# Kernel optimization log

Hardware: AMD Instinct MI355X
Metric: run time of the kernel (lower is better)

Reference implementation:

```python
import jax, jax.numpy as jnp
import numpy as np

NUM_HEADS = 16
WINDOW = 128  # local-attention half-width used by the mask generator
NEG_INF = -1e9


def setup_inputs() -> dict:
    key = jax.random.key(0)
    ks = jax.random.split(key, 12)
    T, N, C = 2048, 2, 1024
    s = 1.0 / np.sqrt(C)
    inp = {
        "q": jax.random.normal(ks[0], (T, N, C), jnp.float32),
        "k": jax.random.normal(ks[1], (T, N, C), jnp.float32),
        "v": jax.random.normal(ks[2], (T, N, C), jnp.float32),
        # MultiHeadDispatch: separate q/k/v input projections + output projection (with bias)
        "Wq": jax.random.normal(ks[3], (C, C), jnp.float32) * s,
        "bq": jnp.zeros((C,), jnp.float32),
        "Wk": jax.random.normal(ks[4], (C, C), jnp.float32) * s,
        "bk": jnp.zeros((C,), jnp.float32),
        "Wv": jax.random.normal(ks[5], (C, C), jnp.float32) * s,
        "bv": jnp.zeros((C,), jnp.float32),
        "Wo": jax.random.normal(ks[6], (C, C), jnp.float32) * s,
        "bo": jnp.zeros((C,), jnp.float32),
        "key_length": jax.random.randint(ks[7], (N,), 1, T, dtype=jnp.int32),
    }
    return inp


def _build_mask(Lq, Lk, key_length):
    # mask_generator: banded local-window mask, True = attend
    i = jnp.arange(Lq)[:, None]
    j = jnp.arange(Lk)[None, :]
    local = jnp.abs(i - j) <= WINDOW                      # (Lq, Lk)
    # forward(): mask[i, :, :key_length[i]] = 1  -> unmask prefix keys per batch elem
    prefix = j[None, :, :] < key_length[:, None, None]    # (N, Lq, Lk)
    return local[None, :, :] | prefix                     # (N, Lq, Lk) bool


def reference(q, k, v, Wq, bq, Wk, bk, Wv, bv, Wo, bo, key_length):
    T, N, C = q.shape
    H = NUM_HEADS
    Dh = C // H
    mask = _build_mask(q.shape[0], k.shape[0], key_length)  # (N, Lq, Lk)

    def heads(x, W, b):
        # (T, N, C) -> project -> (N, H, T, Dh)
        y = x @ W.T + b
        return jnp.transpose(y.reshape(x.shape[0], N, H, Dh), (1, 2, 0, 3))

    qh = heads(q, Wq, bq)
    kh = heads(k, Wk, bk)
    vh = heads(v, Wv, bv)

    scale = 1.0 / np.sqrt(Dh).astype(np.float32)
    scores = jnp.einsum('nhqd,nhkd->nhqk', qh, kh) * scale  # (N, H, Lq, Lk)
    scores = jnp.where(mask[:, None, :, :], scores, NEG_INF)
    att = jax.nn.softmax(scores, axis=-1)
    y = jnp.einsum('nhqk,nhkd->nhqd', att, vh)              # (N, H, Lq, Dh)
    y = jnp.transpose(y, (2, 0, 1, 3)).reshape(T, N, C)     # back to (t, n, c)
    return y @ Wo.T + bo
```

## Files before the change

### kernel.cpp

```cpp
#include <hip/hip_runtime.h>
#include <math.h>

#define T_DIM 2048
#define N_B   2
#define C_DIM 1024
#define H_DIM 16
#define DH    64
#define M_DIM 4096
#define WIN   128

typedef _Float16 h8 __attribute__((ext_vector_type(8)));
typedef float    f4 __attribute__((ext_vector_type(4)));

#if __has_builtin(__builtin_amdgcn_exp2f)
#define EXP2(x) __builtin_amdgcn_exp2f(x)
#else
#define EXP2(x) __expf((x) * 0.693147180559945f)
#endif

__device__ __forceinline__ void glds16(const _Float16* g, _Float16* l) {
    typedef const __attribute__((address_space(1))) unsigned int guint;
    typedef __attribute__((address_space(3))) unsigned int luint;
    __builtin_amdgcn_global_load_lds((guint*)g, (luint*)l, 16, 0, 0);
}

struct CvtA { const float* s; _Float16* d; int n; };
struct Cvt7 { CvtA a[7]; };

__global__ __launch_bounds__(256) void cvt_k(Cvt7 c) {
    CvtA A = c.a[blockIdx.y];
    const int i = (blockIdx.x * 256 + threadIdx.x) * 8;
    if (i >= A.n) return;
    const float4 v0 = *(const float4*)&A.s[i];
    const float4 v1 = *(const float4*)&A.s[i + 4];
    h8 o;
    o[0] = (_Float16)v0.x; o[1] = (_Float16)v0.y;
    o[2] = (_Float16)v0.z; o[3] = (_Float16)v0.w;
    o[4] = (_Float16)v1.x; o[5] = (_Float16)v1.y;
    o[6] = (_Float16)v1.z; o[7] = (_Float16)v1.w;
    *(h8*)&A.d[i] = o;
}

struct QkvArgs {
    const _Float16* x[3];
    const _Float16* w[3];
    const float*    b[3];
    _Float16*       out[3];
};

__global__ __launch_bounds__(256) void proj_qkv(QkvArgs args) {
    const int z = blockIdx.z;
    const _Float16* __restrict__ A = args.x[z];
    const _Float16* __restrict__ B = args.w[z];
    const float* __restrict__ bias = args.b[z];
    _Float16* __restrict__ out     = args.out[z];

    __shared__ _Float16 Sm[3][6144];
    _Float16* smf = &Sm[0][0];

    const int tid  = threadIdx.x;
    const int lane = tid & 63;
    const int wave = tid >> 6;
    const int wr = wave >> 1, wc = wave & 1;
    const int l15 = lane & 15, hi = lane >> 4;
    const int m0 = blockIdx.x << 6;
    const int o0 = blockIdx.y << 7;

    auto STAGE = [&](int b, int k0) {
        {
            const int chunk = tid;
            const int row = chunk >> 2, c4 = chunk & 3;
            const int sc = (c4 ^ ((row >> 1) & 3)) << 3;
            glds16(&A[(size_t)(m0 + row) * C_DIM + k0 + sc], &Sm[b][chunk << 3]);
        }
#pragma unroll
        for (int c = 0; c < 2; ++c) {
            const int chunk = tid + c * 256;
            const int row = chunk >> 2, c4 = chunk & 3;
            const int sc = (c4 ^ ((row >> 1) & 3)) << 3;
            glds16(&B[(size_t)(o0 + row) * C_DIM + k0 + sc],
                   &Sm[b][2048 + (chunk << 3)]);
        }
    };

    f4 acc[2][4];
    const f4 z4 = {0.f, 0.f, 0.f, 0.f};
#pragma unroll
    for (int i = 0; i < 2; ++i)
#pragma unroll
        for (int j = 0; j < 4; ++j) acc[i][j] = z4;

    STAGE(0, 0);
    STAGE(1, 32);
    int buf = 0;
    for (int k0 = 0; k0 < C_DIM; k0 += 32) {
        if (k0 + 32 < C_DIM) {
            asm volatile("s_waitcnt vmcnt(3)" ::: "memory");
        } else {
            asm volatile("s_waitcnt vmcnt(0)" ::: "memory");
        }
        __builtin_amdgcn_s_barrier();
        __builtin_amdgcn_sched_barrier(0);
        if (k0 + 64 < C_DIM) {
            const int nb = (buf + 2 >= 3) ? buf - 1 : buf + 2;
            STAGE(nb, k0 + 64);
        }

        h8 a[2], b[4];
#pragma unroll
        for (int mr = 0; mr < 2; ++mr) {
            const int R = wr * 32 + mr * 16 + l15;
            a[mr] = *(const h8*)&Sm[buf][R * 32 + ((hi ^ ((R >> 1) & 3)) << 3)];
        }
#pragma unroll
        for (int nf = 0; nf < 4; ++nf) {
            const int R = wc * 64 + nf * 16 + l15;
            b[nf] = *(const h8*)&Sm[buf][2048 + R * 32 + ((hi ^ ((R >> 1) & 3)) << 3)];
        }
#pragma unroll
        for (int mr = 0; mr < 2; ++mr)
#pragma unroll
            for (int nf = 0; nf < 4; ++nf)
                acc[mr][nf] = __builtin_amdgcn_mfma_f32_16x16x32_f16(
                    a[mr], b[nf], acc[mr][nf], 0, 0, 0);

        buf = (buf + 1 >= 3) ? 0 : buf + 1;
    }

    __syncthreads();
    const int hh = (o0 >> 6) + wc;
    if (z == 2) {
        _Float16* ws = smf + wave * 3072;
#pragma unroll
        for (int nf = 0; nf < 4; ++nf) {
            const float bb = bias[o0 + wc * 64 + nf * 16 + l15];
            const int d = nf * 16 + l15;
#pragma unroll
            for (int mr = 0; mr < 2; ++mr)
#pragma unroll
                for (int reg = 0; reg < 4; ++reg) {
                    const int ml = mr * 16 + 4 * hi + reg;
                    ws[((ml & 1) * 64 + d) * 24 + (ml >> 1)] =
                        (_Float16)(acc[mr][nf][reg] + bb);
                }
        }
        const int tbase = (m0 + wr * 32) >> 1;
#pragma unroll
        for (int it = 0; it < 4; ++it) {
            const int c = lane + it * 64;
            const int rowi = c >> 1;
            const int th = (c & 1) << 3;
            const h8 v = *(const h8*)&ws[rowi * 24 + th];
            const int n = rowi >> 6, d = rowi & 63;
            *(h8*)&out[((size_t)((n * 16 + hh) * 64 + d)) * T_DIM + tbase + th] = v;
        }
    } else {
        _Float16* ws = smf + wave * 2304;
#pragma unroll
        for (int nf = 0; nf < 4; ++nf) {
            const float bb = bias[o0 + wc * 64 + nf * 16 + l15];
#pragma unroll
            for (int mr = 0; mr < 2; ++mr)
#pragma unroll
                for (int reg = 0; reg < 4; ++reg)
                    ws[(mr * 16 + 4 * hi + reg) * 72 + nf * 16 + l15] =
                        (_Float16)(acc[mr][nf][reg] + bb);
        }
        const int t0 = (m0 + wr * 32) >> 1;
#pragma unroll
        for (int it = 0; it < 4; ++it) {
            const int c = lane + it * 64;
            const int nn = c >> 7;
            const int tq = (c >> 3) & 15;
            const int d8 = (c & 7) << 3;
            const int ml = (tq << 1) | nn;
            const h8 v = *(const h8*)&ws[ml * 72 + d8];
            *(h8*)&out[((size_t)(nn * 16 + hh) * T_DIM + t0 + tq) * DH + d8] = v;
        }
    }
}

__global__ __launch_bounds__(256) void proj_o(
    const _Float16* __restrict__ A, const _Float16* __restrict__ B,
    const float* __restrict__ bias, float* __restrict__ out)
{
    __shared__ _Float16 Sm[3][6144];
    _Float16* smf = &Sm[0][0];

    const int tid  = threadIdx.x;
    const int lane = tid & 63;
    const int wave = tid >> 6;
    const int wr = wave >> 1, wc = wave & 1;
    const int l15 = lane & 15, hi = lane >> 4;
    const int m0 = blockIdx.x << 6;
    const int o0 = blockIdx.y << 7;

    auto STAGE = [&](int b, int k0) {
        {
            const int chunk = tid;
            const int row = chunk >> 2, c4 = chunk & 3;
            const int sc = (c4 ^ ((row >> 1) & 3)) << 3;
            glds16(&A[(size_t)(m0 + row) * C_DIM + k0 + sc], &Sm[b][chunk << 3]);
        }
#pragma unroll
        for (int c = 0; c < 2; ++c) {
            const int chunk = tid + c * 256;
            const int row = chunk >> 2, c4 = chunk & 3;
            const int sc = (c4 ^ ((row >> 1) & 3)) << 3;
            glds16(&B[(size_t)(o0 + row) * C_DIM + k0 + sc],
                   &Sm[b][2048 + (chunk << 3)]);
        }
    };

    f4 acc[2][4];
    const f4 z4 = {0.f, 0.f, 0.f, 0.f};
#pragma unroll
    for (int i = 0; i < 2; ++i)
#pragma unroll
        for (int j = 0; j < 4; ++j) acc[i][j] = z4;

    STAGE(0, 0);
    STAGE(1, 32);
    int buf = 0;
    for (int k0 = 0; k0 < C_DIM; k0 += 32) {
        if (k0 + 32 < C_DIM) {
            asm volatile("s_waitcnt vmcnt(3)" ::: "memory");
        } else {
            asm volatile("s_waitcnt vmcnt(0)" ::: "memory");
        }
        __builtin_amdgcn_s_barrier();
        __builtin_amdgcn_sched_barrier(0);
        if (k0 + 64 < C_DIM) {
            const int nb = (buf + 2 >= 3) ? buf - 1 : buf + 2;
            STAGE(nb, k0 + 64);
        }

        h8 a[2], b[4];
#pragma unroll
        for (int mr = 0; mr < 2; ++mr) {
            const int R = wr * 32 + mr * 16 + l15;
            a[mr] = *(const h8*)&Sm[buf][R * 32 + ((hi ^ ((R >> 1) & 3)) << 3)];
        }
#pragma unroll
        for (int nf = 0; nf < 4; ++nf) {
            const int R = wc * 64 + nf * 16 + l15;
            b[nf] = *(const h8*)&Sm[buf][2048 + R * 32 + ((hi ^ ((R >> 1) & 3)) << 3)];
        }
#pragma unroll
        for (int mr = 0; mr < 2; ++mr)
#pragma unroll
            for (int nf = 0; nf < 4; ++nf)
                acc[mr][nf] = __builtin_amdgcn_mfma_f32_16x16x32_f16(
                    a[mr], b[nf], acc[mr][nf], 0, 0, 0);

        buf = (buf + 1 >= 3) ? 0 : buf + 1;
    }

    __syncthreads();
    float* wsf = (float*)smf + wave * 2176;
#pragma unroll
    for (int nf = 0; nf < 4; ++nf) {
        const float bb = bias[o0 + wc * 64 + nf * 16 + l15];
#pragma unroll
        for (int mr = 0; mr < 2; ++mr)
#pragma unroll
            for (int reg = 0; reg < 4; ++reg)
                wsf[(mr * 16 + 4 * hi + reg) * 68 + nf * 16 + l15] =
                    acc[mr][nf][reg] + bb;
    }
#pragma unroll
    for (int it = 0; it < 8; ++it) {
        const int c = lane + it * 64;
        const int ml = c >> 4;
        const int o4 = (c & 15) << 2;
        const f4 v = *(const f4*)&wsf[ml * 68 + o4];
        *(f4*)&out[(size_t)(m0 + wr * 32 + ml) * C_DIM + o0 + wc * 64 + o4] = v;
    }
}

__global__ __launch_bounds__(256, 2) void attn_v7(
    const _Float16* __restrict__ QH, const _Float16* __restrict__ KH,
    const _Float16* __restrict__ VT, const int* __restrict__ key_length,
    _Float16* __restrict__ Y)
{
    __shared__ _Float16 Ks[2][64 * 64];
    __shared__ _Float16 Vs[2][64 * 64];
    __shared__ _Float16 Ps[4][32 * 72];

    const int nh = blockIdx.x;
    const int n  = nh >> 4;
    const int h  = nh & 15;
    const int qb = blockIdx.y << 7;
    const int kl = key_length[n];
    const int tid  = threadIdx.x;
    const int wave = tid >> 6;
    const int lane = tid & 63;
    const int l15 = lane & 15, hi = lane >> 4;
    const int qw = qb + wave * 32;
    const int swz = l15 & 7;

    const size_t hb = (size_t)nh * T_DIM * DH;
    const _Float16* Qb = QH + hb;
    const _Float16* Kb = KH + hb;
    const _Float16* Vb = VT + hb;

    const int klc0 = ((kl + 63) >> 6) << 6;
    const int klc  = (klc0 < T_DIM) ? klc0 : T_DIM;
    const int blo  = (qb >= WIN) ? ((qb - WIN) & ~63) : 0;
    int bhi = ((qb + 127 + WIN) >> 6) << 6;
    if (bhi > T_DIM - 64) bhi = T_DIM - 64;
    auto nxt = [&](int k0) -> int {
        k0 += 64;
        if (k0 < klc) return k0;
        if (k0 < blo) k0 = blo;
        return (k0 <= bhi) ? k0 : -1;
    };

    auto STAGE = [&](int b, int k0) {
#pragma unroll
        for (int c = 0; c < 2; ++c) {
            const int slot = wave * 128 + c * 64 + lane;
            const int r = slot >> 3, c16 = slot & 7;
            const int sc = (c16 ^ (r & 7)) << 3;
            glds16(&Kb[(size_t)(k0 + r) * DH + sc], &Ks[b][slot << 3]);
        }
#pragma unroll
        for (int c = 0; c < 2; ++c) {
            const int slot = wave * 128 + c * 64 + lane;
            const int r = slot >> 3, c16 = slot & 7;
            const int sc = (c16 ^ (r & 7)) << 3;
            glds16(&Vb[(size_t)r * T_DIM + k0 + sc], &Vs[b][slot << 3]);
        }
    };

    h8 qa[2][2];
#pragma unroll
    for (int mr = 0; mr < 2; ++mr)
#pragma unroll
        for (int ks = 0; ks < 2; ++ks)
            qa[mr][ks] = *(const h8*)&Qb[(size_t)(qw + mr * 16 + l15) * DH + ks * 32 + hi * 8];

    f4 O[2][4];
    const f4 z4 = {0.f, 0.f, 0.f, 0.f};
#pragma unroll
    for (int mr = 0; mr < 2; ++mr)
#pragma unroll
        for (int df = 0; df < 4; ++df) O[mr][df] = z4;
    float m_i[2][4], lp[2][4];
#pragma unroll
    for (int mr = 0; mr < 2; ++mr)
#pragma unroll
        for (int r = 0; r < 4; ++r) { m_i[mr][r] = -1e30f; lp[mr][r] = 0.f; }

    const float SC = 0.18033688f;

    auto TILE = [&](int b, int k0) {
        h8 kb[2][4];
#pragma unroll
        for (int ks = 0; ks < 2; ++ks)
#pragma unroll
            for (int cf = 0; cf < 4; ++cf)
                kb[ks][cf] = *(const h8*)&Ks[b][(cf * 16 + l15) * 64 +
                                                (((ks * 4 + hi) ^ swz) << 3)];

        f4 sacc[2][4];
#pragma unroll
        for (int mr = 0; mr < 2; ++mr)
#pragma unroll
            for (int cf = 0; cf < 4; ++cf) sacc[mr][cf] = z4;
#pragma unroll
        for (int ks = 0; ks < 2; ++ks)
#pragma unroll
            for (int mr = 0; mr < 2; ++mr)
#pragma unroll
                for (int cf = 0; cf < 4; ++cf)
                    sacc[mr][cf] = __builtin_amdgcn_mfma_f32_16x16x32_f16(
                        qa[mr][ks], kb[ks][cf], sacc[mr][cf], 0, 0, 0);

        h8 vb[2][4];
#pragma unroll
        for (int ks = 0; ks < 2; ++ks)
#pragma unroll
            for (int df = 0; df < 4; ++df)
                vb[ks][df] = *(const h8*)&Vs[b][(df * 16 + l15) * 64 +
                                                (((ks * 4 + hi) ^ swz) << 3)];

        const bool full = (k0 + 63 < kl) ||
                          (k0 >= qw + 31 - WIN && k0 + 63 <= qw + WIN);

#pragma unroll
        for (int mr = 0; mr < 2; ++mr) {
            if (full) {
#pragma unroll
                for (int cf = 0; cf < 4; ++cf)
#pragma unroll
                    for (int reg = 0; reg < 4; ++reg)
                        sacc[mr][cf][reg] *= SC;
            } else {
#pragma unroll
                for (int cf = 0; cf < 4; ++cf)
#pragma unroll
                    for (int reg = 0; reg < 4; ++reg) {
                        const int i = qw + mr * 16 + 4 * hi + reg;
                        const int j = k0 + cf * 16 + l15;
                        const int dd = i - j;
                        const bool ok = (dd <= WIN && dd >= -WIN) || (j < kl);
                        sacc[mr][cf][reg] = ok ? sacc[mr][cf][reg] * SC : -1e9f;
                    }
            }
        }

        float lm[2][4];
        bool need = false;
#pragma unroll
        for (int mr = 0; mr < 2; ++mr)
#pragma unroll
            for (int reg = 0; reg < 4; ++reg) {
                lm[mr][reg] = fmaxf(fmaxf(sacc[mr][0][reg], sacc[mr][1][reg]),
                                    fmaxf(sacc[mr][2][reg], sacc[mr][3][reg]));
                need = need || (lm[mr][reg] > m_i[mr][reg]);
            }
        if (__any(need)) {
#pragma unroll
            for (int mr = 0; mr < 2; ++mr)
#pragma unroll
                for (int reg = 0; reg < 4; ++reg) {
                    float mt = lm[mr][reg];
                    mt = fmaxf(mt, __shfl_xor(mt, 1));
                    mt = fmaxf(mt, __shfl_xor(mt, 2));
                    mt = fmaxf(mt, __shfl_xor(mt, 4));
                    mt = fmaxf(mt, __shfl_xor(mt, 8));
                    const float mnew = fmaxf(m_i[mr][reg], mt + 3.0f);
                    const float rr = EXP2(m_i[mr][reg] - mnew);
                    m_i[mr][reg] = mnew;
                    lp[mr][reg] *= rr;
#pragma unroll
                    for (int df = 0; df < 4; ++df) O[mr][df][reg] *= rr;
                }
        }

        _Float16* Pw = &Ps[wave][0];
#pragma unroll
        for (int mr = 0; mr < 2; ++mr)
#pragma unroll
            for (int reg = 0; reg < 4; ++reg) {
                const int row = mr * 16 + 4 * hi + reg;
                const float mi = m_i[mr][reg];
                float acc = 0.f;
#pragma unroll
                for (int cf = 0; cf < 4; ++cf) {
                    const float p = EXP2(sacc[mr][cf][reg] - mi);
                    acc += p;
                    Pw[row * 72 + cf * 16 + l15] = (_Float16)p;
                }
                lp[mr][reg] += acc;
            }

        h8 pa[2][2];
#pragma unroll
        for (int mr = 0; mr < 2; ++mr)
#pragma unroll
            for (int ks = 0; ks < 2; ++ks)
                pa[mr][ks] = *(const h8*)&Pw[(mr * 16 + l15) * 72 + ks * 32 + hi * 8];
#pragma unroll
        for (int ks = 0; ks < 2; ++ks)
#pragma unroll
            for (int mr = 0; mr < 2; ++mr)
#pragma unroll
                for (int df = 0; df < 4; ++df)
                    O[mr][df] = __builtin_amdgcn_mfma_f32_16x16x32_f16(
                        pa[mr][ks], vb[ks][df], O[mr][df], 0, 0, 0);
    };

    STAGE(0, 0);
    __syncthreads();
    int buf = 0, k0 = 0, k1 = nxt(0);
    for (;;) {
        if (k1 >= 0) STAGE(buf ^ 1, k1);
        const bool wkeep = (k0 < kl) || (k0 <= qw + 31 + WIN && k0 + 63 >= qw - WIN);
        if (wkeep) TILE(buf, k0);
        __syncthreads();
        if (k1 < 0) break;
        k0 = k1; k1 = nxt(k0); buf ^= 1;
    }

    float lf[2][4];
#pragma unroll
    for (int mr = 0; mr < 2; ++mr)
#pragma unroll
        for (int reg = 0; reg < 4; ++reg) {
            float l = lp[mr][reg];
            l += __shfl_xor(l, 1); l += __shfl_xor(l, 2);
            l += __shfl_xor(l, 4); l += __shfl_xor(l, 8);
            lf[mr][reg] = l;
        }

#pragma unroll
    for (int mr = 0; mr < 2; ++mr)
#pragma unroll
        for (int reg = 0; reg < 4; ++reg) {
            const float inv = 1.f / lf[mr][reg];
            const int i = qw + mr * 16 + 4 * hi + reg;
#pragma unroll
            for (int df = 0; df < 4; ++df) {
                Y[((size_t)i * N_B + n) * C_DIM + h * DH + df * 16 + l15] =
                    (_Float16)(O[mr][df][reg] * inv);
            }
        }
}

extern "C" void kernel_launch(void* const* d_in, const int* in_sizes, int n_in,
                              void* d_out, int out_size, void* d_ws, size_t ws_size,
                              hipStream_t stream) {
    const float* q  = (const float*)d_in[0];
    const float* k  = (const float*)d_in[1];
    const float* v  = (const float*)d_in[2];
    const float* Wq = (const float*)d_in[3];
    const float* bq = (const float*)d_in[4];
    const float* Wk = (const float*)d_in[5];
    const float* bk = (const float*)d_in[6];
    const float* Wv = (const float*)d_in[7];
    const float* bv = (const float*)d_in[8];
    const float* Wo = (const float*)d_in[9];
    const float* bo = (const float*)d_in[10];
    const int*   kl = (const int*)d_in[11];

    const int NX = M_DIM * C_DIM;
    const int NW = C_DIM * C_DIM;

    _Float16* xq = (_Float16*)d_ws;
    _Float16* xk = xq + NX;
    _Float16* xv = xk + NX;
    _Float16* wq = xv + NX;
    _Float16* wk = wq + NW;
    _Float16* wv = wk + NW;
    _Float16* wo = wv + NW;
    _Float16* QHh = wo + NW;
    _Float16* KHh = QHh + NX;
    _Float16* VTh = KHh + NX;
    _Float16* Yh  = xq;

    Cvt7 c;
    c.a[0] = {q,  xq, NX}; c.a[1] = {k,  xk, NX}; c.a[2] = {v,  xv, NX};
    c.a[3] = {Wq, wq, NW}; c.a[4] = {Wk, wk, NW};
    c.a[5] = {Wv, wv, NW}; c.a[6] = {Wo, wo, NW};
    cvt_k<<<dim3(NX / (256 * 8), 7), 256, 0, stream>>>(c);

    QkvArgs qa;
    qa.x[0] = xq; qa.x[1] = xk; qa.x[2] = xv;
    qa.w[0] = wq; qa.w[1] = wk; qa.w[2] = wv;
    qa.b[0] = bq; qa.b[1] = bk; qa.b[2] = bv;
    qa.out[0] = QHh; qa.out[1] = KHh; qa.out[2] = VTh;
    proj_qkv<<<dim3(M_DIM / 64, C_DIM / 128, 3), 256, 0, stream>>>(qa);

    attn_v7<<<dim3(N_B * H_DIM, T_DIM / 128), 256, 0, stream>>>(QHh, KHh, VTh, kl, Yh);

    proj_o<<<dim3(M_DIM / 64, C_DIM / 128), 256, 0, stream>>>(Yh, wo, bo, (float*)d_out);
}
```

Before: 110.0 us.

## Fuse fp32-to-fp16 conversion into projection GEMM loaders, drop convert kernel

Removes the separate conversion kernel that turned the fp32 activations and weights into fp16 copies in workspace. The projection GEMMs now load fp32 tiles into registers, convert them, and write them to LDS with a register-staged double buffer, replacing the async global-to-LDS triple buffer. This avoids a full extra read and write pass over the inputs and one kernel launch. In exchange the GEMMs read twice as many bytes per operand, re-convert each weight tile for every M-tile block, and give up the direct-to-LDS async loads, which may expose more load latency.

```diff
diff --git a/kernel.cpp b/kernel.cpp
--- a/kernel.cpp
+++ b/kernel.cpp
@@ -24,38 +24,30 @@
     __builtin_amdgcn_global_load_lds((guint*)g, (luint*)l, 16, 0, 0);
 }
 
-struct CvtA { const float* s; _Float16* d; int n; };
-struct Cvt7 { CvtA a[7]; };
-
-__global__ __launch_bounds__(256) void cvt_k(Cvt7 c) {
-    CvtA A = c.a[blockIdx.y];
-    const int i = (blockIdx.x * 256 + threadIdx.x) * 8;
-    if (i >= A.n) return;
-    const float4 v0 = *(const float4*)&A.s[i];
-    const float4 v1 = *(const float4*)&A.s[i + 4];
+__device__ __forceinline__ h8 cvt8(const float4 a, const float4 b) {
     h8 o;
-    o[0] = (_Float16)v0.x; o[1] = (_Float16)v0.y;
-    o[2] = (_Float16)v0.z; o[3] = (_Float16)v0.w;
-    o[4] = (_Float16)v1.x; o[5] = (_Float16)v1.y;
-    o[6] = (_Float16)v1.z; o[7] = (_Float16)v1.w;
-    *(h8*)&A.d[i] = o;
+    o[0] = (_Float16)a.x; o[1] = (_Float16)a.y;
+    o[2] = (_Float16)a.z; o[3] = (_Float16)a.w;
+    o[4] = (_Float16)b.x; o[5] = (_Float16)b.y;
+    o[6] = (_Float16)b.z; o[7] = (_Float16)b.w;
+    return o;
 }
 
 struct QkvArgs {
-    const _Float16* x[3];
-    const _Float16* w[3];
-    const float*    b[3];
-    _Float16*       out[3];
+    const float* x[3];
+    const float* w[3];
+    const float* b[3];
+    _Float16*    out[3];
 };
 
 __global__ __launch_bounds__(256) void proj_qkv(QkvArgs args) {
     const int z = blockIdx.z;
-    const _Float16* __restrict__ A = args.x[z];
-    const _Float16* __restrict__ B = args.w[z];
+    const float* __restrict__ A = args.x[z];
+    const float* __restrict__ B = args.w[z];
     const float* __restrict__ bias = args.b[z];
     _Float16* __restrict__ out     = args.out[z];
 
-    __shared__ _Float16 Sm[3][6144];
+    __shared__ _Float16 Sm[2][6144];
     _Float16* smf = &Sm[0][0];
 
     const int tid  = threadIdx.x;
@@ -66,21 +58,23 @@
     const int m0 = blockIdx.x << 6;
     const int o0 = blockIdx.y << 7;
 
-    auto STAGE = [&](int b, int k0) {
-        {
-            const int chunk = tid;
-            const int row = chunk >> 2, c4 = chunk & 3;
-            const int sc = (c4 ^ ((row >> 1) & 3)) << 3;
-            glds16(&A[(size_t)(m0 + row) * C_DIM + k0 + sc], &Sm[b][chunk << 3]);
-        }
-#pragma unroll
-        for (int c = 0; c < 2; ++c) {
-            const int chunk = tid + c * 256;
-            const int row = chunk >> 2, c4 = chunk & 3;
-            const int sc = (c4 ^ ((row >> 1) & 3)) << 3;
-            glds16(&B[(size_t)(o0 + row) * C_DIM + k0 + sc],
-                   &Sm[b][2048 + (chunk << 3)]);
-        }
+    const int rowA = tid >> 2, a4 = tid & 3;
+    const int sw = ((a4 ^ ((rowA >> 1) & 3)) << 3);
+
+    float4 ra0, ra1, rb0, rb1, rb2, rb3;
+
+    auto LOADR = [&](int k0) {
+        const float* pa = &A[(size_t)(m0 + rowA) * C_DIM + k0 + a4 * 8];
+        ra0 = *(const float4*)pa; ra1 = *(const float4*)(pa + 4);
+        const float* pb0 = &B[(size_t)(o0 + rowA) * C_DIM + k0 + a4 * 8];
+        rb0 = *(const float4*)pb0; rb1 = *(const float4*)(pb0 + 4);
+        const float* pb1 = &B[(size_t)(o0 + 64 + rowA) * C_DIM + k0 + a4 * 8];
+        rb2 = *(const float4*)pb1; rb3 = *(const float4*)(pb1 + 4);
+    };
+    auto WRITE = [&](int b) {
+        *(h8*)&Sm[b][rowA * 32 + sw]               = cvt8(ra0, ra1);
+        *(h8*)&Sm[b][2048 + rowA * 32 + sw]        = cvt8(rb0, rb1);
+        *(h8*)&Sm[b][2048 + (64 + rowA) * 32 + sw] = cvt8(rb2, rb3);
     };
 
     f4 acc[2][4];
@@ -90,21 +84,17 @@
 #pragma unroll
         for (int j = 0; j < 4; ++j) acc[i][j] = z4;
 
-    STAGE(0, 0);
-    STAGE(1, 32);
+    LOADR(0);
+    WRITE(0);
+    LOADR(32);
+    asm volatile("s_waitcnt lgkmcnt(0)" ::: "memory");
+    __builtin_amdgcn_s_barrier();
+    __builtin_amdgcn_sched_barrier(0);
+
     int buf = 0;
     for (int k0 = 0; k0 < C_DIM; k0 += 32) {
-        if (k0 + 32 < C_DIM) {
-            asm volatile("s_waitcnt vmcnt(3)" ::: "memory");
-        } else {
-            asm volatile("s_waitcnt vmcnt(0)" ::: "memory");
-        }
-        __builtin_amdgcn_s_barrier();
-        __builtin_amdgcn_sched_barrier(0);
-        if (k0 + 64 < C_DIM) {
-            const int nb = (buf + 2 >= 3) ? buf - 1 : buf + 2;
-            STAGE(nb, k0 + 64);
-        }
+        if (k0 + 32 < C_DIM) WRITE(buf ^ 1);
+        if (k0 + 64 < C_DIM) LOADR(k0 + 64);
 
         h8 a[2], b[4];
 #pragma unroll
@@ -124,7 +114,10 @@
                 acc[mr][nf] = __builtin_amdgcn_mfma_f32_16x16x32_f16(
                     a[mr], b[nf], acc[mr][nf], 0, 0, 0);
 
-        buf = (buf + 1 >= 3) ? 0 : buf + 1;
+        asm volatile("s_waitcnt lgkmcnt(0)" ::: "memory");
+        __builtin_amdgcn_s_barrier();
+        __builtin_amdgcn_sched_barrier(0);
+        buf ^= 1;
     }
 
     __syncthreads();
@@ -181,7 +174,7 @@
 }
 
 __global__ __launch_bounds__(256) void proj_o(
-    const _Float16* __restrict__ A, const _Float16* __restrict__ B,
+    const _Float16* __restrict__ A, const float* __restrict__ B,
     const float* __restrict__ bias, float* __restrict__ out)
 {
     __shared__ _Float16 Sm[3][6144];
@@ -195,21 +188,23 @@
     const int m0 = blockIdx.x << 6;
     const int o0 = blockIdx.y << 7;
 
-    auto STAGE = [&](int b, int k0) {
-        {
-            const int chunk = tid;
-            const int row = chunk >> 2, c4 = chunk & 3;
-            const int sc = (c4 ^ ((row >> 1) & 3)) << 3;
-            glds16(&A[(size_t)(m0 + row) * C_DIM + k0 + sc], &Sm[b][chunk << 3]);
-        }
-#pragma unroll
-        for (int c = 0; c < 2; ++c) {
-            const int chunk = tid + c * 256;
-            const int row = chunk >> 2, c4 = chunk & 3;
-            const int sc = (c4 ^ ((row >> 1) & 3)) << 3;
-            glds16(&B[(size_t)(o0 + row) * C_DIM + k0 + sc],
-                   &Sm[b][2048 + (chunk << 3)]);
-        }
+    const int rowA = tid >> 2, a4 = tid & 3;
+    const int sw = ((a4 ^ ((rowA >> 1) & 3)) << 3);
+
+    h8 ya;
+    float4 rb0, rb1, rb2, rb3;
+
+    auto LOADR = [&](int k0) {
+        ya = *(const h8*)&A[(size_t)(m0 + rowA) * C_DIM + k0 + a4 * 8];
+        const float* pb0 = &B[(size_t)(o0 + rowA) * C_DIM + k0 + a4 * 8];
+        rb0 = *(const float4*)pb0; rb1 = *(const float4*)(pb0 + 4);
+        const float* pb1 = &B[(size_t)(o0 + 64 + rowA) * C_DIM + k0 + a4 * 8];
+        rb2 = *(const float4*)pb1; rb3 = *(const float4*)(pb1 + 4);
+    };
+    auto WRITE = [&](int b) {
+        *(h8*)&Sm[b][rowA * 32 + sw]               = ya;
+        *(h8*)&Sm[b][2048 + rowA * 32 + sw]        = cvt8(rb0, rb1);
+        *(h8*)&Sm[b][2048 + (64 + rowA) * 32 + sw] = cvt8(rb2, rb3);
     };
 
     f4 acc[2][4];
@@ -219,21 +214,17 @@
 #pragma unroll
         for (int j = 0; j < 4; ++j) acc[i][j] = z4;
 
-    STAGE(0, 0);
-    STAGE(1, 32);
+    LOADR(0);
+    WRITE(0);
+    LOADR(32);
+    asm volatile("s_waitcnt lgkmcnt(0)" ::: "memory");
+    __builtin_amdgcn_s_barrier();
+    __builtin_amdgcn_sched_barrier(0);
+
     int buf = 0;
     for (int k0 = 0; k0 < C_DIM; k0 += 32) {
-        if (k0 + 32 < C_DIM) {
-            asm volatile("s_waitcnt vmcnt(3)" ::: "memory");
-        } else {
-            asm volatile("s_waitcnt vmcnt(0)" ::: "memory");
-        }
-        __builtin_amdgcn_s_barrier();
-        __builtin_amdgcn_sched_barrier(0);
-        if (k0 + 64 < C_DIM) {
-            const int nb = (buf + 2 >= 3) ? buf - 1 : buf + 2;
-            STAGE(nb, k0 + 64);
-        }
+        if (k0 + 32 < C_DIM) WRITE(buf ^ 1);
+        if (k0 + 64 < C_DIM) LOADR(k0 + 64);
 
         h8 a[2], b[4];
 #pragma unroll
@@ -253,7 +244,10 @@
                 acc[mr][nf] = __builtin_amdgcn_mfma_f32_16x16x32_f16(
                     a[mr], b[nf], acc[mr][nf], 0, 0, 0);
 
-        buf = (buf + 1 >= 3) ? 0 : buf + 1;
+        asm volatile("s_waitcnt lgkmcnt(0)" ::: "memory");
+        __builtin_amdgcn_s_barrier();
+        __builtin_amdgcn_sched_barrier(0);
+        buf ^= 1;
     }
 
     __syncthreads();
@@ -526,34 +520,20 @@
     const int*   kl = (const int*)d_in[11];
 
     const int NX = M_DIM * C_DIM;
-    const int NW = C_DIM * C_DIM;
-
-    _Float16* xq = (_Float16*)d_ws;
-    _Float16* xk = xq + NX;
-    _Float16* xv = xk + NX;
-    _Float16* wq = xv + NX;
-    _Float16* wk = wq + NW;
-    _Float16* wv = wk + NW;
-    _Float16* wo = wv + NW;
-    _Float16* QHh = wo + NW;
+
+    _Float16* QHh = (_Float16*)d_ws;
     _Float16* KHh = QHh + NX;
     _Float16* VTh = KHh + NX;
-    _Float16* Yh  = xq;
-
-    Cvt7 c;
-    c.a[0] = {q,  xq, NX}; c.a[1] = {k,  xk, NX}; c.a[2] = {v,  xv, NX};
-    c.a[3] = {Wq, wq, NW}; c.a[4] = {Wk, wk, NW};
-    c.a[5] = {Wv, wv, NW}; c.a[6] = {Wo, wo, NW};
-    cvt_k<<<dim3(NX / (256 * 8), 7), 256, 0, stream>>>(c);
+    _Float16* Yh  = VTh + NX;
 
     QkvArgs qa;
-    qa.x[0] = xq; qa.x[1] = xk; qa.x[2] = xv;
-    qa.w[0] = wq; qa.w[1] = wk; qa.w[2] = wv;
+    qa.x[0] = q;  qa.x[1] = k;  qa.x[2] = v;
+    qa.w[0] = Wq; qa.w[1] = Wk; qa.w[2] = Wv;
     qa.b[0] = bq; qa.b[1] = bk; qa.b[2] = bv;
     qa.out[0] = QHh; qa.out[1] = KHh; qa.out[2] = VTh;
     proj_qkv<<<dim3(M_DIM / 64, C_DIM / 128, 3), 256, 0, stream>>>(qa);
 
     attn_v7<<<dim3(N_B * H_DIM, T_DIM / 128), 256, 0, stream>>>(QHh, KHh, VTh, kl, Yh);
 
-    proj_o<<<dim3(M_DIM / 64, C_DIM / 128), 256, 0, stream>>>(Yh, wo, bo, (float*)d_out);
+    proj_o<<<dim3(M_DIM / 64, C_DIM / 128), 256, 0, stream>>>(Yh, Wo, bo, (float*)d_out);
 }
```

After: 110.6 us. No clear change (+0.6%).
